# Performance work log

Measured on AMD Instinct MI355X. Metric: run time of the kernel, lower is better.

## Reference

```python
import jax, jax.numpy as jnp
import numpy as np

NV = 100000   # vehicle nodes
NE = 100000   # 'edge' nodes (dst type)
E = 250000    # graph edges (connects relation)
VDIM = 16
EDIM = 16
HID = 128
HEADS = 4
DH = 128      # out_feats per head (GATv2Conv(hid, hid))
EPS = 1e-5
NEG_SLOPE = 0.2


def _layernorm(x, g, b):
    mu = x.mean(-1, keepdims=True)
    var = ((x - mu) ** 2).mean(-1, keepdims=True)
    return (x - mu) * jax.lax.rsqrt(var + EPS) * g + b


def setup_inputs() -> dict:
    key = jax.random.key(0)
    ks = jax.random.split(key, 20)
    s = 0.05
    return {
        "v_feat": jax.random.normal(ks[0], (NV, VDIM), jnp.float32),
        "e_feat": jax.random.normal(ks[1], (NE, EDIM), jnp.float32),
        "Wv": jax.random.normal(ks[2], (VDIM, HID), jnp.float32) * s,
        "bv": jnp.zeros((HID,), jnp.float32),
        "gv": jnp.ones((HID,), jnp.float32),
        "betav": jnp.zeros((HID,), jnp.float32),
        "We": jax.random.normal(ks[3], (EDIM, HID), jnp.float32) * s,
        "be": jnp.zeros((HID,), jnp.float32),
        "ge": jnp.ones((HID,), jnp.float32),
        "betae": jnp.zeros((HID,), jnp.float32),
        "Wsrc": jax.random.normal(ks[4], (HID, HEADS * DH), jnp.float32) * s,
        "bsrc": jnp.zeros((HEADS * DH,), jnp.float32),
        "Wdst": jax.random.normal(ks[5], (HID, HEADS * DH), jnp.float32) * s,
        "bdst": jnp.zeros((HEADS * DH,), jnp.float32),
        "attn": jax.random.normal(ks[6], (HEADS, DH), jnp.float32) * s,
        "Wp": jax.random.normal(ks[7], (HID, HID), jnp.float32) * s,
        "bp": jnp.zeros((HID,), jnp.float32),
        "src": jax.random.randint(ks[8], (E,), 0, NV, jnp.int32),
        "dst": jax.random.randint(ks[9], (E,), 0, NE, jnp.int32),
    }


def reference(v_feat, e_feat, Wv, bv, gv, betav, We, be, ge, betae,
              Wsrc, bsrc, Wdst, bdst, attn, Wp, bp, src, dst):
    # --- node-type encoders: Linear -> ReLU -> LayerNorm ---
    h_v = _layernorm(jax.nn.relu(v_feat @ Wv + bv), gv, betav)      # [NV, HID]
    h_e = _layernorm(jax.nn.relu(e_feat @ We + be), ge, betae)      # [NE, HID]

    # --- GATv2Conv (bipartite: vehicle -> edge), 4 heads ---
    fs = (h_v @ Wsrc + bsrc).reshape(NV, HEADS, DH)                 # src proj
    fd = (h_e @ Wdst + bdst).reshape(NE, HEADS, DH)                 # dst proj
    e = jax.nn.leaky_relu(fs[src] + fd[dst], NEG_SLOPE)             # [E, H, D]
    score = jnp.einsum("ehd,hd->eh", e, attn)                       # [E, H]
    # segment-wise (per-dst-node) softmax over incoming edges
    smax = jax.ops.segment_max(score, dst, num_segments=NE)         # [NE, H]
    ex = jnp.exp(score - smax[dst])
    denom = jax.ops.segment_sum(ex, dst, num_segments=NE)
    alpha = ex / denom[dst]                                         # [E, H]
    out = jax.ops.segment_sum(alpha[:, :, None] * fs[src], dst,
                              num_segments=NE)                      # [NE, H, D]

    # HeteroGraphConv mean-aggregate (single relation -> identity),
    # then mean over heads (edge_out.dim()==3 branch)
    edge_out = out.mean(axis=1)                                     # [NE, HID]

    # feature_proj: Linear -> ReLU -> Dropout(eval: identity)
    return jax.nn.relu(edge_out @ Wp + bp)
```

## Files before the change

### kernel.cpp

```cpp
#include <hip/hip_runtime.h>
#include <hip/hip_bf16.h>
#include <math.h>

#define NV 100000
#define NE_N 100000
#define NEDGE 250000
#define NPAD 100096
#define NEG 0.2f
#define LN_EPS 1e-5f

typedef __bf16 bf16_t;
typedef __bf16 bf16x8 __attribute__((ext_vector_type(8)));
typedef float f32x4 __attribute__((ext_vector_type(4)));
typedef float f32x2 __attribute__((ext_vector_type(2)));

__device__ inline unsigned short f2bfu(float f) {
    return __builtin_bit_cast(unsigned short, (__bf16)f);
}
__device__ inline float blo(unsigned w) { return __uint_as_float(w << 16); }
__device__ inline float bhi(unsigned w) { return __uint_as_float(w & 0xffff0000u); }
__device__ inline float lrelu(float x) { return x > 0.f ? x : NEG * x; }
__device__ inline unsigned pk2(float a, float b) {
    return (unsigned)f2bfu(a) | ((unsigned)f2bfu(b) << 16);
}

__device__ __forceinline__ void gload_lds16(const void* g, void* l) {
    __builtin_amdgcn_global_load_lds(
        (const __attribute__((address_space(1))) unsigned int*)g,
        (__attribute__((address_space(3))) unsigned int*)l,
        16, 0, 0);
}

__global__ __launch_bounds__(256) void prep_kernel(
    const float* __restrict__ Wsrc, const float* __restrict__ Wdst,
    const float* __restrict__ Wp, bf16_t* __restrict__ pS,
    bf16_t* __restrict__ pD, bf16_t* __restrict__ pP,
    int* __restrict__ deg)
{
    int t = blockIdx.x * 256 + threadIdx.x;
    if (t < 8192) {
        int ksq = t >> 9, col = t & 511;
#pragma unroll
        for (int j = 0; j < 8; ++j)
            pS[(size_t)t * 8 + j] = (bf16_t)Wsrc[(ksq * 8 + j) * 512 + col];
    } else if (t < 16384) {
        int g = t - 8192;
        int ksq = g >> 9, col = g & 511;
#pragma unroll
        for (int j = 0; j < 8; ++j)
            pD[(size_t)g * 8 + j] = (bf16_t)Wdst[(ksq * 8 + j) * 512 + col];
    } else if (t < 18432) {
        int g = t - 16384;
        int ksq = g >> 7, col = g & 127;
#pragma unroll
        for (int j = 0; j < 8; ++j)
            pP[(size_t)g * 8 + j] = (bf16_t)Wp[(ksq * 8 + j) * 128 + col];
    } else {
        int z = t - 18432;
        if (z < NE_N) deg[z] = 0;
    }
}

__global__ __launch_bounds__(256) void count_kernel(
    const int* __restrict__ dst, int* __restrict__ deg)
{
    int t = blockIdx.x * 256 + threadIdx.x;
    if (t < NEDGE) atomicAdd(&deg[dst[t]], 1);
}

__global__ __launch_bounds__(256) void scan1_kernel(
    const int* __restrict__ deg, int* __restrict__ offs, int* __restrict__ bsum)
{
    __shared__ int s[256];
    int i = blockIdx.x * 256 + threadIdx.x;
    int v = (i < NE_N) ? deg[i] : 0;
    s[threadIdx.x] = v;
    __syncthreads();
    for (int off = 1; off < 256; off <<= 1) {
        int t_ = (threadIdx.x >= off) ? s[threadIdx.x - off] : 0;
        __syncthreads();
        s[threadIdx.x] += t_;
        __syncthreads();
    }
    if (i < NE_N) offs[i] = s[threadIdx.x] - v;
    if (threadIdx.x == 255) bsum[blockIdx.x] = s[255];
}

__global__ __launch_bounds__(512) void scan2_kernel(int* __restrict__ bsum, int nb)
{
    __shared__ int s[512];
    int t = threadIdx.x;
    int v = (t < nb) ? bsum[t] : 0;
    s[t] = v;
    __syncthreads();
    for (int off = 1; off < 512; off <<= 1) {
        int t_ = (t >= off) ? s[t - off] : 0;
        __syncthreads();
        s[t] += t_;
        __syncthreads();
    }
    if (t < nb) bsum[t] = s[t] - v;
}

__global__ __launch_bounds__(256) void scan3_kernel(
    int* __restrict__ offs, const int* __restrict__ bsum, int* __restrict__ cursor)
{
    int i = blockIdx.x * 256 + threadIdx.x;
    if (i < NE_N) {
        int o = offs[i] + bsum[blockIdx.x];
        offs[i] = o;
        cursor[i] = o;
    }
}

__global__ __launch_bounds__(256) void scatter_kernel(
    const int* __restrict__ dst, int* __restrict__ cursor, int* __restrict__ eidx)
{
    int t = blockIdx.x * 256 + threadIdx.x;
    if (t < NEDGE) {
        int pos = atomicAdd(&cursor[dst[t]], 1);
        eidx[pos] = t;
    }
}

__global__ __launch_bounds__(512, 4) void enc_proj_kernel(
    const float* __restrict__ featV, const float* __restrict__ WencV,
    const float* __restrict__ bencV, const float* __restrict__ gV,
    const float* __restrict__ betaV, const bf16_t* __restrict__ ApackV,
    const float* __restrict__ bprojV, unsigned short* __restrict__ outV,
    const float* __restrict__ featE, const float* __restrict__ WencE,
    const float* __restrict__ bencE, const float* __restrict__ gE,
    const float* __restrict__ betaE, const bf16_t* __restrict__ ApackE,
    const float* __restrict__ bprojE, unsigned short* __restrict__ outE,
    int nblk1, int M)
{
    __shared__ unsigned short Hs[128 * 136];
    __shared__ __align__(16) unsigned short Abuf[2][8192];
    __shared__ __align__(16) float Bias[512];

    int b = blockIdx.x;
    bool isV = b < nblk1;
    const float* feat  = isV ? featV  : featE;
    const float* Wenc  = isV ? WencV  : WencE;
    const float* benc  = isV ? bencV  : bencE;
    const float* gln   = isV ? gV     : gE;
    const float* beta  = isV ? betaV  : betaE;
    const bf16_t* Apack = isV ? ApackV : ApackE;
    const float* bproj = isV ? bprojV : bprojE;
    unsigned short* out = isV ? outV : outE;
    int row0 = (isV ? b : b - nblk1) * 128;

    int t = threadIdx.x;
    int l = t & 63;
    int w = t >> 6;
    int rbase = __builtin_amdgcn_readfirstlane(w * 16);

    {
        int sr = row0 + rbase + (l >> 2);
        if (sr > M - 1) sr = M - 1;
        gload_lds16(feat + (size_t)sr * 16 + (l & 3) * 4, &Abuf[1][w * 512]);
    }

#pragma unroll
    for (int j = 0; j < 2; ++j) {
        int ksq = w * 2 + j;
        gload_lds16(Apack + ((size_t)(ksq * 512) + l) * 8, &Abuf[0][ksq * 512]);
    }
    if (t < 128)
        *(float4*)&Bias[t * 4] = *(const float4*)(bproj + t * 4);

    f32x2 wc2[16];
#pragma unroll
    for (int k = 0; k < 16; ++k) {
        float2 wv = *(const float2*)(Wenc + k * 128 + 2 * l);
        wc2[k][0] = wv.x;
        wc2[k][1] = wv.y;
    }
    float2 bv2 = *(const float2*)(benc + 2 * l);

    asm volatile("s_waitcnt vmcnt(0)" ::: "memory");

    const float* Fs = (const float*)&Abuf[1][0];
#pragma unroll
    for (int i = 0; i < 16; ++i) {
        const float* fr = Fs + (rbase + i) * 16;
        float4 f0 = *(const float4*)(fr);
        float4 f1 = *(const float4*)(fr + 4);
        float4 f2 = *(const float4*)(fr + 8);
        float4 f3 = *(const float4*)(fr + 12);
        f32x2 a = {bv2.x, bv2.y};
        a = __builtin_elementwise_fma((f32x2)f0.x, wc2[0],  a);
        a = __builtin_elementwise_fma((f32x2)f0.y, wc2[1],  a);
        a = __builtin_elementwise_fma((f32x2)f0.z, wc2[2],  a);
        a = __builtin_elementwise_fma((f32x2)f0.w, wc2[3],  a);
        a = __builtin_elementwise_fma((f32x2)f1.x, wc2[4],  a);
        a = __builtin_elementwise_fma((f32x2)f1.y, wc2[5],  a);
        a = __builtin_elementwise_fma((f32x2)f1.z, wc2[6],  a);
        a = __builtin_elementwise_fma((f32x2)f1.w, wc2[7],  a);
        a = __builtin_elementwise_fma((f32x2)f2.x, wc2[8],  a);
        a = __builtin_elementwise_fma((f32x2)f2.y, wc2[9],  a);
        a = __builtin_elementwise_fma((f32x2)f2.z, wc2[10], a);
        a = __builtin_elementwise_fma((f32x2)f2.w, wc2[11], a);
        a = __builtin_elementwise_fma((f32x2)f3.x, wc2[12], a);
        a = __builtin_elementwise_fma((f32x2)f3.y, wc2[13], a);
        a = __builtin_elementwise_fma((f32x2)f3.z, wc2[14], a);
        a = __builtin_elementwise_fma((f32x2)f3.w, wc2[15], a);
        float a0 = fmaxf(a[0], 0.f);
        float a1 = fmaxf(a[1], 0.f);
        *(unsigned*)&Hs[(rbase + i) * 136 + 2 * l] = pk2(a0, a1);
    }

    float s = 0.f, s2 = 0.f;
    {
        int rr = rbase + (l >> 2);
        int q = l & 3;
#pragma unroll
        for (int j = 0; j < 4; ++j) {
            uint4 v = *(const uint4*)&Hs[rr * 136 + q * 32 + j * 8];
            float x;
            x = blo(v.x); s += x; s2 = fmaf(x, x, s2);
            x = bhi(v.x); s += x; s2 = fmaf(x, x, s2);
            x = blo(v.y); s += x; s2 = fmaf(x, x, s2);
            x = bhi(v.y); s += x; s2 = fmaf(x, x, s2);
            x = blo(v.z); s += x; s2 = fmaf(x, x, s2);
            x = bhi(v.z); s += x; s2 = fmaf(x, x, s2);
            x = blo(v.w); s += x; s2 = fmaf(x, x, s2);
            x = bhi(v.w); s += x; s2 = fmaf(x, x, s2);
        }
    }
    s  += __shfl_xor(s, 1, 64);  s  += __shfl_xor(s, 2, 64);
    s2 += __shfl_xor(s2, 1, 64); s2 += __shfl_xor(s2, 2, 64);
    float mu  = s * (1.f / 128.f);
    float var = s2 * (1.f / 128.f) - mu * mu;
    float inv = rsqrtf(var + LN_EPS);

    int kq = l >> 4;
    int ln = l & 15;
    float mu_r  = __shfl(mu,  ln * 4, 64);
    float inv_r = __shfl(inv, ln * 4, 64);

    bf16x8 bfr[4];
#pragma unroll
    for (int ks = 0; ks < 4; ++ks) {
        int c0 = ks * 32 + kq * 8;
        uint4 v = *(const uint4*)&Hs[(rbase + ln) * 136 + c0];
        float4 g0 = *(const float4*)(gln + c0);
        float4 g1 = *(const float4*)(gln + c0 + 4);
        float4 b0 = *(const float4*)(beta + c0);
        float4 b1 = *(const float4*)(beta + c0 + 4);
        uint4 p;
        p.x = pk2(fmaf((blo(v.x) - mu_r) * inv_r, g0.x, b0.x),
                  fmaf((bhi(v.x) - mu_r) * inv_r, g0.y, b0.y));
        p.y = pk2(fmaf((blo(v.y) - mu_r) * inv_r, g0.z, b0.z),
                  fmaf((bhi(v.y) - mu_r) * inv_r, g0.w, b0.w));
        p.z = pk2(fmaf((blo(v.z) - mu_r) * inv_r, g1.x, b1.x),
                  fmaf((bhi(v.z) - mu_r) * inv_r, g1.y, b1.y));
        p.w = pk2(fmaf((blo(v.w) - mu_r) * inv_r, g1.z, b1.z),
                  fmaf((bhi(v.w) - mu_r) * inv_r, g1.w, b1.w));
        bfr[ks] = __builtin_bit_cast(bf16x8, p);
    }

    unsigned short* stag = Hs + rbase * 136;
    int node = row0 + rbase + ln;

#pragma unroll
    for (int p = 0; p < 8; ++p) {
        if (p == 0)
            asm volatile("s_waitcnt lgkmcnt(0)" ::: "memory");
        else
            asm volatile("s_waitcnt vmcnt(2)" ::: "memory");
        __builtin_amdgcn_s_barrier();

        if (p < 7) {
#pragma unroll
            for (int j = 0; j < 2; ++j) {
                int ksq = w * 2 + j;
                gload_lds16(Apack + ((size_t)(ksq * 512 + (p + 1) * 64) + l) * 8,
                            &Abuf[(p + 1) & 1][ksq * 512]);
            }
            __builtin_amdgcn_sched_barrier(0);
        }

        const unsigned short* Ac = Abuf[p & 1];
#pragma unroll
        for (int mt = 0; mt < 4; ++mt) {
            bf16x8 a[4];
#pragma unroll
            for (int ks = 0; ks < 4; ++ks)
                a[ks] = *(const bf16x8*)&Ac[((ks * 4 + kq) * 64 + mt * 16 + ln) * 8];

            f32x4 acc = {0.f, 0.f, 0.f, 0.f};
#pragma unroll
            for (int ks = 0; ks < 4; ++ks)
                acc = __builtin_amdgcn_mfma_f32_16x16x32_bf16(a[ks], bfr[ks], acc, 0, 0, 0);

            int colp = p * 64 + mt * 16 + kq * 4;
            float4 bb = *(const float4*)&Bias[colp];
            ushort4 o;
            o.x = f2bfu(acc[0] + bb.x);
            o.y = f2bfu(acc[1] + bb.y);
            o.z = f2bfu(acc[2] + bb.z);
            o.w = f2bfu(acc[3] + bb.w);
            *(ushort4*)&stag[ln * 136 + mt * 16 + kq * 4] = o;
        }
#pragma unroll
        for (int i = 0; i < 2; ++i) {
            uint4 v = *(const uint4*)&stag[ln * 136 + i * 32 + kq * 8];
            *(uint4*)(out + (size_t)node * 512 + p * 64 + i * 32 + kq * 8) = v;
        }
    }
}

__global__ __launch_bounds__(256) void final_gemm_kernel(
    const float* __restrict__ A, const unsigned short* __restrict__ Abf,
    const bf16_t* __restrict__ Ppack, const float* __restrict__ bp,
    float* __restrict__ C, int M)
{
    __shared__ unsigned short Hs[64 * 136];
    int t = threadIdx.x;
    int lane = t & 63;
    int w = t >> 6;
    int row0 = blockIdx.x * 64;

    if (Abf) {
#pragma unroll
        for (int i = 0; i < 4; ++i) {
            int idx = i * 256 + t;
            int r = idx >> 4;
            int c = (idx & 15) * 8;
            uint4 v = make_uint4(0, 0, 0, 0);
            if (row0 + r < M)
                v = *(const uint4*)(Abf + (size_t)(row0 + r) * 128 + c);
            *(uint4*)&Hs[r * 136 + c] = v;
        }
    } else {
#pragma unroll
        for (int i = 0; i < 8; ++i) {
            int f4 = i * 256 + t;
            int r = f4 >> 5;
            int c4 = (f4 & 31) * 4;
            float4 v = make_float4(0.f, 0.f, 0.f, 0.f);
            if (row0 + r < M)
                v = ((const float4*)(A + (size_t)(row0 + r) * 128))[f4 & 31];
            ushort4 o;
            o.x = f2bfu(v.x); o.y = f2bfu(v.y); o.z = f2bfu(v.z); o.w = f2bfu(v.w);
            *(ushort4*)&Hs[r * 136 + c4] = o;
        }
    }
    __syncthreads();

    int kq = lane >> 4;
    int ln = lane & 15;

    f32x4 acc[2][4];
#pragma unroll
    for (int mt = 0; mt < 2; ++mt)
#pragma unroll
        for (int nt = 0; nt < 4; ++nt) {
            f32x4 z = {0.f, 0.f, 0.f, 0.f};
            acc[mt][nt] = z;
        }

#pragma unroll
    for (int ks = 0; ks < 4; ++ks) {
        bf16x8 bfr[4];
#pragma unroll
        for (int nt = 0; nt < 4; ++nt) {
            const uint4* p = (const uint4*)&Hs[(nt * 16 + ln) * 136 + ks * 32 + kq * 8];
            bfr[nt] = __builtin_bit_cast(bf16x8, *p);
        }
        bf16x8 afr[2];
#pragma unroll
        for (int mt = 0; mt < 2; ++mt) {
            int colA = w * 32 + mt * 16 + ln;
            afr[mt] = *(const bf16x8*)(Ppack + ((size_t)(ks * 4 + kq) * 128 + colA) * 8);
        }
#pragma unroll
        for (int mt = 0; mt < 2; ++mt)
#pragma unroll
            for (int nt = 0; nt < 4; ++nt)
                acc[mt][nt] = __builtin_amdgcn_mfma_f32_16x16x32_bf16(
                    afr[mt], bfr[nt], acc[mt][nt], 0, 0, 0);
    }

#pragma unroll
    for (int mt = 0; mt < 2; ++mt) {
        int col = w * 32 + mt * 16 + kq * 4;
        float4 bb = *(const float4*)(bp + col);
#pragma unroll
        for (int nt = 0; nt < 4; ++nt) {
            int node = row0 + nt * 16 + ln;
            if (node < M) {
                float4 o;
                o.x = fmaxf(acc[mt][nt][0] + bb.x, 0.f);
                o.y = fmaxf(acc[mt][nt][1] + bb.y, 0.f);
                o.z = fmaxf(acc[mt][nt][2] + bb.z, 0.f);
                o.w = fmaxf(acc[mt][nt][3] + bb.w, 0.f);
                *(float4*)(C + (size_t)node * 128 + col) = o;
            }
        }
    }
}

__global__ __launch_bounds__(256) void softagg_kernel(
    const unsigned short* __restrict__ fs, const unsigned short* __restrict__ fdp,
    const float* __restrict__ attn, const int* __restrict__ src,
    const int* __restrict__ offs, const int* __restrict__ deg,
    const int* __restrict__ eidx, float* __restrict__ outf,
    unsigned short* __restrict__ eo)
{
    int d = blockIdx.x * 4 + (threadIdx.x >> 6);
    if (d >= NE_N) return;
    int l = threadIdx.x & 63;
    int r0 = offs[d];
    int n = deg[d];
    int o = l * 8;

    uint4 fv = *(const uint4*)(fdp + (size_t)d * 512 + o);
    float fdv[8] = { blo(fv.x), bhi(fv.x), blo(fv.y), bhi(fv.y),
                     blo(fv.z), bhi(fv.z), blo(fv.w), bhi(fv.w) };
    float4 w0 = *(const float4*)(attn + o);
    float4 w1 = *(const float4*)(attn + o + 4);
    float wv[8] = { w0.x, w0.y, w0.z, w0.w, w1.x, w1.y, w1.z, w1.w };

    float m = -1e30f, sm = 0.f;
    float acc[8];
#pragma unroll
    for (int j = 0; j < 8; ++j) acc[j] = 0.f;

    for (int base = 0; base < n; base += 64) {
        int cnt = min(n - base, 64);
        int sl = 0;
        if (l < cnt) sl = src[eidx[r0 + base + l]];
        for (int i = 0; i < cnt; ++i) {
            int s = __shfl(sl, i, 64);
            uint4 a = *(const uint4*)(fs + (size_t)s * 512 + o);
            float fsv[8] = { blo(a.x), bhi(a.x), blo(a.y), bhi(a.y),
                             blo(a.z), bhi(a.z), blo(a.w), bhi(a.w) };
            float p = 0.f;
#pragma unroll
            for (int j = 0; j < 8; ++j)
                p = fmaf(lrelu(fsv[j] + fdv[j]), wv[j], p);
#pragma unroll
            for (int mk = 1; mk < 16; mk <<= 1)
                p += __shfl_xor(p, mk, 64);
            float mn = fmaxf(m, p);
            float c  = __expf(m - mn);
            float av = __expf(p - mn);
            sm = sm * c + av;
            m = mn;
#pragma unroll
            for (int j = 0; j < 8; ++j)
                acc[j] = fmaf(av, fsv[j], acc[j] * c);
        }
    }

    float inv = (n > 0) ? 0.25f / sm : 0.f;
#pragma unroll
    for (int j = 0; j < 8; ++j) {
        float v = acc[j] * inv;
        v += __shfl_xor(v, 16, 64);
        v += __shfl_xor(v, 32, 64);
        acc[j] = v;
    }
    if (l < 16) {
        if (eo) {
            uint4 pk;
            pk.x = pk2(acc[0], acc[1]);
            pk.y = pk2(acc[2], acc[3]);
            pk.z = pk2(acc[4], acc[5]);
            pk.w = pk2(acc[6], acc[7]);
            *(uint4*)(eo + (size_t)d * 128 + l * 8) = pk;
        } else {
            float4 o0 = make_float4(acc[0], acc[1], acc[2], acc[3]);
            float4 o1 = make_float4(acc[4], acc[5], acc[6], acc[7]);
            *(float4*)(outf + (size_t)d * 128 + l * 8) = o0;
            *(float4*)(outf + (size_t)d * 128 + l * 8 + 4) = o1;
        }
    }
}

extern "C" void kernel_launch(void* const* d_in, const int* in_sizes, int n_in,
                              void* d_out, int out_size, void* d_ws, size_t ws_size,
                              hipStream_t stream)
{
    const float* v_feat = (const float*)d_in[0];
    const float* e_feat = (const float*)d_in[1];
    const float* Wv     = (const float*)d_in[2];
    const float* bv     = (const float*)d_in[3];
    const float* gv     = (const float*)d_in[4];
    const float* betav  = (const float*)d_in[5];
    const float* We     = (const float*)d_in[6];
    const float* be     = (const float*)d_in[7];
    const float* ge     = (const float*)d_in[8];
    const float* betae  = (const float*)d_in[9];
    const float* Wsrc   = (const float*)d_in[10];
    const float* bsrc   = (const float*)d_in[11];
    const float* Wdst   = (const float*)d_in[12];
    const float* bdst   = (const float*)d_in[13];
    const float* attn   = (const float*)d_in[14];
    const float* Wp     = (const float*)d_in[15];
    const float* bp     = (const float*)d_in[16];
    const int*   src    = (const int*)d_in[17];
    const int*   dst    = (const int*)d_in[18];
    float* out = (float*)d_out;

    unsigned short* fs = (unsigned short*)d_ws;
    unsigned short* fd = fs + (size_t)NPAD * 512;
    int* deg    = (int*)(fd + (size_t)NPAD * 512);
    int* offs   = deg + NE_N;
    int* cursor = offs + NE_N;
    int* bsum   = cursor + NE_N;
    int* eidx   = bsum + 512;
    bf16_t* pS  = (bf16_t*)(eidx + NEDGE);
    bf16_t* pD  = pS + 65536;
    bf16_t* pP  = pD + 65536;
    unsigned short* eo = (unsigned short*)(pP + 16384);

    size_t need = (size_t)((char*)(eo + (size_t)NE_N * 128) - (char*)d_ws);
    if (ws_size < need) eo = nullptr;

    const int NB_SCAN = (NE_N + 255) / 256;

    prep_kernel<<<463, 256, 0, stream>>>(Wsrc, Wdst, Wp, pS, pD, pP, deg);

    count_kernel<<<(NEDGE + 255) / 256, 256, 0, stream>>>(dst, deg);
    scan1_kernel<<<NB_SCAN, 256, 0, stream>>>(deg, offs, bsum);
    scan2_kernel<<<1, 512, 0, stream>>>(bsum, NB_SCAN);
    scan3_kernel<<<NB_SCAN, 256, 0, stream>>>(offs, bsum, cursor);
    scatter_kernel<<<(NEDGE + 255) / 256, 256, 0, stream>>>(dst, cursor, eidx);

    enc_proj_kernel<<<1564, 512, 0, stream>>>(
        v_feat, Wv, bv, gv, betav, pS, bsrc, fs,
        e_feat, We, be, ge, betae, pD, bdst, fd,
        782, 100000);

    softagg_kernel<<<NE_N / 4, 256, 0, stream>>>(fs, fd, attn, src, offs, deg,
                                                 eidx, out, eo);

    final_gemm_kernel<<<1563, 256, 0, stream>>>(out, eo, pP, bp, out, NE_N);
}
```

Measured before the change: 291.5 us.

## Pre-gather source indices in CSR and shrink encoder-projection tiles to 64 rows

The scatter step now stores the source node id directly in CSR order, so the aggregation kernel reads it in one load instead of a dependent load through an edge index. Offset and degree are packed into a single int2 read per destination. The encoder/projection kernel moves from 128-row, 512-thread blocks to 64-row, 256-thread blocks, roughly doubling the grid to raise occupancy and parallelism, at the cost of loading the packed weights more often overall. Padding shrinks to match the new tile size.

```diff
diff --git a/kernel.cpp b/kernel.cpp
--- a/kernel.cpp
+++ b/kernel.cpp
@@ -5,7 +5,7 @@
 #define NV 100000
 #define NE_N 100000
 #define NEDGE 250000
-#define NPAD 100096
+#define NPAD 100032
 #define NEG 0.2f
 #define LN_EPS 1e-5f
 
@@ -103,27 +103,31 @@
 }
 
 __global__ __launch_bounds__(256) void scan3_kernel(
-    int* __restrict__ offs, const int* __restrict__ bsum, int* __restrict__ cursor)
+    int* __restrict__ offs, const int* __restrict__ bsum,
+    int* __restrict__ cursor, const int* __restrict__ deg,
+    int2* __restrict__ od)
 {
     int i = blockIdx.x * 256 + threadIdx.x;
     if (i < NE_N) {
         int o = offs[i] + bsum[blockIdx.x];
         offs[i] = o;
         cursor[i] = o;
+        od[i] = make_int2(o, deg[i]);
     }
 }
 
 __global__ __launch_bounds__(256) void scatter_kernel(
-    const int* __restrict__ dst, int* __restrict__ cursor, int* __restrict__ eidx)
+    const int* __restrict__ dst, const int* __restrict__ src,
+    int* __restrict__ cursor, int* __restrict__ srcs)
 {
     int t = blockIdx.x * 256 + threadIdx.x;
     if (t < NEDGE) {
         int pos = atomicAdd(&cursor[dst[t]], 1);
-        eidx[pos] = t;
-    }
-}
-
-__global__ __launch_bounds__(512, 4) void enc_proj_kernel(
+        srcs[pos] = src[t];
+    }
+}
+
+__global__ __launch_bounds__(256, 4) void enc_proj_kernel(
     const float* __restrict__ featV, const float* __restrict__ WencV,
     const float* __restrict__ bencV, const float* __restrict__ gV,
     const float* __restrict__ betaV, const bf16_t* __restrict__ ApackV,
@@ -134,7 +138,7 @@
     const float* __restrict__ bprojE, unsigned short* __restrict__ outE,
     int nblk1, int M)
 {
-    __shared__ unsigned short Hs[128 * 136];
+    __shared__ unsigned short Hs[64 * 136];
     __shared__ __align__(16) unsigned short Abuf[2][8192];
     __shared__ __align__(16) float Bias[512];
 
@@ -148,7 +152,7 @@
     const bf16_t* Apack = isV ? ApackV : ApackE;
     const float* bproj = isV ? bprojV : bprojE;
     unsigned short* out = isV ? outV : outE;
-    int row0 = (isV ? b : b - nblk1) * 128;
+    int row0 = (isV ? b : b - nblk1) * 64;
 
     int t = threadIdx.x;
     int l = t & 63;
@@ -162,8 +166,8 @@
     }
 
 #pragma unroll
-    for (int j = 0; j < 2; ++j) {
-        int ksq = w * 2 + j;
+    for (int j = 0; j < 4; ++j) {
+        int ksq = w * 4 + j;
         gload_lds16(Apack + ((size_t)(ksq * 512) + l) * 8, &Abuf[0][ksq * 512]);
     }
     if (t < 128)
@@ -273,8 +277,8 @@
 
         if (p < 7) {
 #pragma unroll
-            for (int j = 0; j < 2; ++j) {
-                int ksq = w * 2 + j;
+            for (int j = 0; j < 4; ++j) {
+                int ksq = w * 4 + j;
                 gload_lds16(Apack + ((size_t)(ksq * 512 + (p + 1) * 64) + l) * 8,
                             &Abuf[(p + 1) & 1][ksq * 512]);
             }
@@ -404,16 +408,16 @@
 
 __global__ __launch_bounds__(256) void softagg_kernel(
     const unsigned short* __restrict__ fs, const unsigned short* __restrict__ fdp,
-    const float* __restrict__ attn, const int* __restrict__ src,
-    const int* __restrict__ offs, const int* __restrict__ deg,
-    const int* __restrict__ eidx, float* __restrict__ outf,
+    const float* __restrict__ attn, const int2* __restrict__ od,
+    const int* __restrict__ srcs, float* __restrict__ outf,
     unsigned short* __restrict__ eo)
 {
     int d = blockIdx.x * 4 + (threadIdx.x >> 6);
     if (d >= NE_N) return;
     int l = threadIdx.x & 63;
-    int r0 = offs[d];
-    int n = deg[d];
+    int2 rd = od[d];
+    int r0 = rd.x;
+    int n  = rd.y;
     int o = l * 8;
 
     uint4 fv = *(const uint4*)(fdp + (size_t)d * 512 + o);
@@ -431,7 +435,7 @@
     for (int base = 0; base < n; base += 64) {
         int cnt = min(n - base, 64);
         int sl = 0;
-        if (l < cnt) sl = src[eidx[r0 + base + l]];
+        if (l < cnt) sl = srcs[r0 + base + l];
         for (int i = 0; i < cnt; ++i) {
             int s = __shfl(sl, i, 64);
             uint4 a = *(const uint4*)(fs + (size_t)s * 512 + o);
@@ -511,8 +515,9 @@
     int* offs   = deg + NE_N;
     int* cursor = offs + NE_N;
     int* bsum   = cursor + NE_N;
-    int* eidx   = bsum + 512;
-    bf16_t* pS  = (bf16_t*)(eidx + NEDGE);
+    int2* od    = (int2*)(bsum + 512);
+    int* srcs   = (int*)(od + NE_N);
+    bf16_t* pS  = (bf16_t*)(srcs + NEDGE);
     bf16_t* pD  = pS + 65536;
     bf16_t* pP  = pD + 65536;
     unsigned short* eo = (unsigned short*)(pP + 16384);
@@ -527,16 +532,16 @@
     count_kernel<<<(NEDGE + 255) / 256, 256, 0, stream>>>(dst, deg);
     scan1_kernel<<<NB_SCAN, 256, 0, stream>>>(deg, offs, bsum);
     scan2_kernel<<<1, 512, 0, stream>>>(bsum, NB_SCAN);
-    scan3_kernel<<<NB_SCAN, 256, 0, stream>>>(offs, bsum, cursor);
-    scatter_kernel<<<(NEDGE + 255) / 256, 256, 0, stream>>>(dst, cursor, eidx);
-
-    enc_proj_kernel<<<1564, 512, 0, stream>>>(
+    scan3_kernel<<<NB_SCAN, 256, 0, stream>>>(offs, bsum, cursor, deg, od);
+    scatter_kernel<<<(NEDGE + 255) / 256, 256, 0, stream>>>(dst, src, cursor, srcs);
+
+    enc_proj_kernel<<<3126, 256, 0, stream>>>(
         v_feat, Wv, bv, gv, betav, pS, bsrc, fs,
         e_feat, We, be, ge, betae, pD, bdst, fd,
-        782, 100000);
-
-    softagg_kernel<<<NE_N / 4, 256, 0, stream>>>(fs, fd, attn, src, offs, deg,
-                                                 eidx, out, eo);
+        1563, 100000);
+
+    softagg_kernel<<<NE_N / 4, 256, 0, stream>>>(fs, fd, attn, od, srcs,
+                                                 out, eo);
 
     final_gemm_kernel<<<1563, 256, 0, stream>>>(out, eo, pP, bp, out, NE_N);
 }
```

Result: no change. 287.0 us (-1.5%).
